# Kernel optimization log

Hardware: AMD Instinct MI355X
Metric: run time of the kernel (lower is better)

## Reference

```python
import jax, jax.numpy as jnp
import numpy as np

N_QUBITS = 10
DEPTH = 2
CNOT_PATTERN = [(i, i + 1) for i in range(N_QUBITS - 1)] + [(N_QUBITS - 1, 0)]

def _signs(n):
    # Pauli-Z eigenvalue (+1/-1) of each basis state for each wire; wire 0 = MSB
    idx = np.arange(2 ** n)
    bits = (idx[:, None] >> np.arange(n - 1, -1, -1)[None, :]) & 1
    return jnp.asarray(1.0 - 2.0 * bits, jnp.float32)  # [2^n, n]

SIGNS = _signs(N_QUBITS)

def _apply_rx(s, theta, wire):
    # s: [B, 2,2,...,2] complex; RX(theta) = [[c, -i s],[-i s, c]], c=cos(theta/2)
    s0 = jnp.take(s, 0, axis=wire + 1)
    s1 = jnp.take(s, 1, axis=wire + 1)
    c = jnp.cos(theta * 0.5)
    sn = jnp.sin(theta * 0.5)
    if c.ndim:  # per-batch angle -> broadcast over remaining wire axes
        shp = (-1,) + (1,) * (s0.ndim - 1)
        c = c.reshape(shp)
        sn = sn.reshape(shp)
    return jnp.stack([c * s0 - 1j * sn * s1, -1j * sn * s0 + c * s1], axis=wire + 1)

def _apply_cnot(s, src, tgt):
    # flip target wire on the src=1 subspace (X gate == flip of the size-2 axis)
    s0 = jnp.take(s, 0, axis=src + 1)
    s1 = jnp.take(s, 1, axis=src + 1)
    t_ax = tgt + 1 - (1 if tgt > src else 0)  # target axis after removing src axis
    s1 = jnp.flip(s1, axis=t_ax)
    return jnp.stack([s0, s1], axis=src + 1)

def _qgate(x, rx_params):
    # x: [B, n_qubits] data angles -> PauliZ expectations [B, n_qubits]
    B = x.shape[0]
    n = N_QUBITS
    s = jnp.zeros((B, 2 ** n), jnp.complex64).at[:, 0].set(1.0)
    s = s.reshape((B,) + (2,) * n)
    for w in range(n):
        s = _apply_rx(s, x[:, w], w)
    for _ in range(DEPTH):
        for w in range(n):
            s = _apply_rx(s, rx_params[w], w)
        for src, tgt in CNOT_PATTERN:
            s = _apply_cnot(s, src, tgt)
    probs = jnp.abs(s.reshape(B, -1)) ** 2  # [B, 2^n]
    return probs @ SIGNS  # [B, n]


def setup_inputs():
    key = jax.random.key(0)
    ks = jax.random.split(key, 10)
    T, B, D, H = 256, 256, 128, N_QUBITS
    fan_in = D + H
    sc = 1.0 / np.sqrt(fan_in)
    def lin(k1, k2):
        W = jax.random.uniform(k1, (H, fan_in), jnp.float32, -sc, sc)
        b = jax.random.uniform(k2, (H,), jnp.float32, -sc, sc)
        return W, b
    inputs = jax.random.normal(ks[0], (T, B, D), jnp.float32)
    rx_params = jax.random.normal(ks[1], (H,), jnp.float32)
    Wf, bf = lin(ks[2], ks[3])
    Wi, bi = lin(ks[4], ks[5])
    Wg, bg = lin(ks[6], ks[7])
    Wo, bo = lin(ks[8], ks[9])
    return dict(inputs=inputs, rx_params=rx_params, Wf=Wf, bf=bf, Wi=Wi, bi=bi,
                Wg=Wg, bg=bg, Wo=Wo, bo=bo)


def reference(inputs, rx_params, Wf, bf, Wi, bi, Wg, bg, Wo, bo):
    T, B, _ = inputs.shape
    H = N_QUBITS
    def step(carry, x_t):
        hx, cx = carry
        comb = jnp.concatenate([x_t, hx], axis=1)  # [B, D+H]
        f = jax.nn.sigmoid(_qgate(comb @ Wf.T + bf, rx_params))
        i = jax.nn.sigmoid(_qgate(comb @ Wi.T + bi, rx_params))
        g = jnp.tanh(_qgate(comb @ Wg.T + bg, rx_params))
        o = jax.nn.sigmoid(_qgate(comb @ Wo.T + bo, rx_params))
        cx = f * cx + i * g
        hx = o * jnp.tanh(cx)
        return (hx, cx), hx
    h0 = jnp.zeros((B, H), inputs.dtype)
    c0 = jnp.zeros((B, H), inputs.dtype)
    (hT, cT), ys = jax.lax.scan(step, (h0, c0), inputs)
    return ys, hT, cT
```

## Files before the change

### kernel.cpp

```cpp
#include <hip/hip_runtime.h>
#include <math.h>

#define T_STEPS 256
#define BATCH   256
#define DDIM    128
#define NH      10

typedef float v2f __attribute__((ext_vector_type(2)));
__device__ __forceinline__ v2f sp(float x){ v2f r; r.x = x; r.y = x; return r; }
#define PKFMA(a,b,c) __builtin_elementwise_fma((a),(b),(c))

template<int CTRL, int RMASK, int BMASK>
__device__ __forceinline__ float dppz(float x){
  return __int_as_float(__builtin_amdgcn_update_dpp(
      0, __float_as_int(x), CTRL, RMASK, BMASK, true));
}
template<int CTRL>
__device__ __forceinline__ float qperm(float x){
  int xi = __float_as_int(x);
  return __int_as_float(__builtin_amdgcn_update_dpp(xi, xi, CTRL, 0xF, 0xF, false));
}
__device__ __forceinline__ float red63(float v){
  v += dppz<0x111, 0xF, 0xF>(v);
  v += dppz<0x112, 0xF, 0xF>(v);
  v += dppz<0x114, 0xF, 0xE>(v);
  v += dppz<0x118, 0xF, 0xC>(v);
  v += dppz<0x142, 0xA, 0xF>(v);
  v += dppz<0x143, 0xC, 0xF>(v);
  return v;
}
__device__ __forceinline__ float rdlane(float v, int l){
  return __int_as_float(__builtin_amdgcn_readlane(__float_as_int(v), l));
}
__device__ __forceinline__ float qp2(float x){ return qperm<0x4E>(x); }
__device__ __forceinline__ float qp1(float x){ return qperm<0xB1>(x); }

template<int CTRL,int RMASK,int BMASK>
__device__ __forceinline__ float lad_add(float v){ return v + dppz<CTRL,RMASK,BMASK>(v); }
template<int CTRL,int RMASK,int BMASK>
__device__ __forceinline__ float lad_sub(float v){ return dppz<CTRL,RMASK,BMASK>(v) - v; }
#define LAD0_A(v) lad_add<0x111,0xF,0xF>(v)
#define LAD0_S(v) lad_sub<0x111,0xF,0xF>(v)
#define LAD1_A(v) lad_add<0x112,0xF,0xF>(v)
#define LAD1_S(v) lad_sub<0x112,0xF,0xF>(v)
#define LAD2_A(v) lad_add<0x114,0xF,0xE>(v)
#define LAD2_S(v) lad_sub<0x114,0xF,0xE>(v)
#define LAD3_A(v) lad_add<0x118,0xF,0xC>(v)
#define LAD3_S(v) lad_sub<0x118,0xF,0xC>(v)
#define LAD4_A(v) lad_add<0x142,0xA,0xF>(v)
#define LAD4_S(v) lad_sub<0x142,0xA,0xF>(v)
#define LAD5_A(v) lad_add<0x143,0xC,0xF>(v)
#define LAD5_S(v) lad_sub<0x143,0xC,0xF>(v)

__device__ __forceinline__ float dsx32(float x){ return __shfl_xor(x, 32, 64); }
__device__ __forceinline__ float dsx16(float x){
  return __int_as_float(__builtin_amdgcn_ds_swizzle(__float_as_int(x), 0x401F));
}
__device__ __forceinline__ float dsx8(float x){
  return __int_as_float(__builtin_amdgcn_ds_swizzle(__float_as_int(x), 0x201F));
}
__device__ __forceinline__ float dsx4(float x){
  return __int_as_float(__builtin_amdgcn_ds_swizzle(__float_as_int(x), 0x101F));
}

#define NK 4

#define RX_LANE_PK(FETCH, cv, sv)                                              \
  { const v2f cc_ = sp(cv), ss_ = sp(sv);                                      \
    _Pragma("unroll")                                                          \
    for (int k = 0; k < NK; ++k){                                              \
      v2f oa, ob;                                                              \
      oa.x = FETCH(RE[k].x); oa.y = FETCH(RE[k].y);                            \
      ob.x = FETCH(IM[k].x); ob.y = FETCH(IM[k].y);                            \
      RE[k] = PKFMA(cc_, RE[k], ss_ * ob);                                     \
      IM[k] = PKFMA(cc_, IM[k], -(ss_ * oa));                                  \
    } }

template<int XB>
__device__ __forceinline__ void rx_reg_pk(float c, float s, v2f* RE, v2f* IM){
  const v2f cc = sp(c), ss = sp(s);
  v2f oR[NK], oI[NK];
  #pragma unroll
  for (int k = 0; k < NK; ++k){ oR[k] = RE[k]; oI[k] = IM[k]; }
  #pragma unroll
  for (int k = 0; k < NK; ++k){
    RE[k] = PKFMA(cc, oR[k],  ss * oI[k ^ XB]);
    IM[k] = PKFMA(cc, oI[k], -(ss * oR[k ^ XB]));
  }
}
__device__ __forceinline__ void rx_reg9_pk(float c, float s, v2f* RE, v2f* IM){
  const v2f cc = sp(c), ss = sp(s);
  #pragma unroll
  for (int k = 0; k < NK; ++k){
    v2f oa = __builtin_shufflevector(RE[k], RE[k], 1, 0);
    v2f ob = __builtin_shufflevector(IM[k], IM[k], 1, 0);
    RE[k] = PKFMA(cc, RE[k],  ss * ob);
    IM[k] = PKFMA(cc, IM[k], -(ss * oa));
  }
}

__device__ __forceinline__ void xdots(float xa, float xb,
                                      const v2f* WA, const v2f* WB, float* s){
  v2f xav = sp(xa), xbv = sp(xb);
  v2f p0 = PKFMA(xav, WA[0], xbv * WB[0]);
  v2f p1 = PKFMA(xav, WA[1], xbv * WB[1]);
  v2f p2 = PKFMA(xav, WA[2], xbv * WB[2]);
  s[0] = red63(p0.x); s[1] = red63(p0.y);
  s[2] = red63(p1.x); s[3] = red63(p1.y);
  s[4] = red63(p2.x);
}

__global__ void __launch_bounds__(512)
__attribute__((amdgpu_waves_per_eu(2)))
qlstm_kernel(const float* __restrict__ inp, const float* __restrict__ rxp,
             const float* __restrict__ Wf, const float* __restrict__ bf,
             const float* __restrict__ Wi, const float* __restrict__ bi,
             const float* __restrict__ Wg, const float* __restrict__ bg,
             const float* __restrict__ Wo, const float* __restrict__ bo,
             float* __restrict__ out)
{
  const int b    = blockIdx.x;
  const int tid  = threadIdx.x;
  const int wv   = tid >> 6;
  const int g    = wv >> 1;
  const int half = wv & 1;
  const int lane = tid & 63;

  __shared__ float4 Sx[4][2][4][64];
  __shared__ float4 partv[2][64];
  __shared__ float xpub_s[4][16];
  ((float*)partv)[tid] = 0.f;

  const float* Wp = (g == 0) ? Wf : (g == 1) ? Wi : (g == 2) ? Wg : Wo;
  const float* bp = (g == 0) ? bf : (g == 1) ? bi : (g == 2) ? bg : bo;

  const float WSC = 0.07957747154594767f;

  const int wbase = half * 5;
  v2f WA[3], WB[3];
  float bq[5];
  #pragma unroll
  for (int k = 0; k < 5; ++k) bq[k] = WSC * (bp[wbase + k] + rxp[wbase + k]);
  #pragma unroll
  for (int j = 0; j < 3; ++j){
    const int w0 = wbase + 2*j, w1 = wbase + 2*j + 1;
    WA[j].x = WSC * Wp[w0*138 + lane];
    WB[j].x = WSC * Wp[w0*138 + 64 + lane];
    if (2*j + 1 < 5){
      WA[j].y = WSC * Wp[w1*138 + lane];
      WB[j].y = WSC * Wp[w1*138 + 64 + lane];
    } else { WA[j].y = 0.f; WB[j].y = 0.f; }
  }
  float wCT[NH];
  {
    const int row = (lane < NH) ? lane : 0;
    #pragma unroll
    for (int j = 0; j < NH; ++j){
      float v = WSC * Wp[row*138 + 128 + j];
      wCT[j] = (lane < NH) ? v : 0.f;
    }
  }

  float pc[NH], ps[NH];
  #pragma unroll
  for (int w = 0; w < NH; ++w){
    float th = 0.5f * rxp[w];
    pc[w] = cosf(th);
    ps[w] = sinf(th);
  }

  const int l5 = (lane>>5)&1, l4 = (lane>>4)&1, l3 = (lane>>3)&1;
  const int l2 = (lane>>2)&1, l1 = (lane>>1)&1, l0 = lane&1;
  const int pb2 = l4^l3, pb3 = l3^l2, pb4 = l2^l1, pb5 = l1^l0;
  const int a0 = l5, a1 = l5^l4;
  const int a6w = l0 ^ half;
  const int n_base = pb2 + pb3 + pb4 + pb5 + a6w;

  v2f CRE[NK], CIM[NK];
  #pragma unroll
  for (int r = 0; r < 2*NK; ++r){
    const int R0 = r&1, R1 = (r>>1)&1, R2 = (r>>2)&1;
    int k = (n_base + (a0^R0) + (a1^R0) + (half^R2) + (R2^R1) + (R1^R0)) & 3;
    float cr = (k==0) ? 1.f : (k==2) ? -1.f : 0.f;
    float ci = (k==1) ? -1.f : (k==3) ? 1.f : 0.f;
    if (R0){ CRE[r>>1].y = cr; CIM[r>>1].y = ci; }
    else   { CRE[r>>1].x = cr; CIM[r>>1].x = ci; }
  }

  const float sig = (lane == 0 || lane >= 6) ? -1.f : 1.f;

  float h = 0.f, c = 0.f;

  const float* x0 = inp + (size_t)b * DDIM;
  float xa = x0[lane];
  float xb = x0[64 + lane];

  {
    float sx[5];
    xdots(xa, xb, WA, WB, sx);
    if (lane == 63){
      #pragma unroll
      for (int k = 0; k < 5; ++k) xpub_s[g][wbase + k] = sx[k] + bq[k];
    }
  }
  __syncthreads();

  #pragma unroll 1
  for (int t = 0; t < T_STEPS; ++t){
    if (t + 1 < T_STEPS){
      const float* nx = inp + ((size_t)(t+1) * BATCH + b) * DDIM;
      xa = nx[lane];
      xb = nx[64 + lane];
    }

    float cs[NH], sn[NH];
    {
      float xr = xpub_s[g][lane & 15];
      float hdA = rdlane(h, 0) * wCT[0];
      float hdB = rdlane(h, 1) * wCT[1];
      hdA = fmaf(rdlane(h, 2), wCT[2], hdA);
      hdB = fmaf(rdlane(h, 3), wCT[3], hdB);
      hdA = fmaf(rdlane(h, 4), wCT[4], hdA);
      hdB = fmaf(rdlane(h, 5), wCT[5], hdB);
      hdA = fmaf(rdlane(h, 6), wCT[6], hdA);
      hdB = fmaf(rdlane(h, 7), wCT[7], hdB);
      hdA = fmaf(rdlane(h, 8), wCT[8], hdA);
      hdB = fmaf(rdlane(h, 9), wCT[9], hdB);
      float th = xr + (hdA + hdB);
      float cA = __builtin_amdgcn_cosf(th);
      float sA = __builtin_amdgcn_sinf(th);
      #pragma unroll
      for (int w = 0; w < NH; ++w){
        cs[w] = rdlane(cA, w);
        sn[w] = rdlane(sA, w);
      }
    }

    float f2 = pb2 ? sn[2] : cs[2];
    float f3 = pb3 ? sn[3] : cs[3];
    float f4 = pb4 ? sn[4] : cs[4];
    float f5 = pb5 ? sn[5] : cs[5];
    float m2345 = ((f2*f3)*(f4*f5)) * (a6w ? sn[6] : cs[6]);

    float q0 = (a0 ? sn[0] : cs[0]) * (a1 ? sn[1] : cs[1]);
    float q1 = (a0 ? cs[0] : sn[0]) * (a1 ? cs[1] : sn[1]);
    v2f ZZ; ZZ.x = m2345 * q0; ZZ.y = m2345 * q1;

    float u7  = half ? sn[7] : cs[7];
    float u7b = half ? cs[7] : sn[7];
    float t78[4];
    t78[0] = u7  * cs[8];
    t78[1] = u7  * sn[8];
    t78[2] = u7b * sn[8];
    t78[3] = u7b * cs[8];

    v2f s9a; s9a.x = cs[9]; s9a.y = sn[9];
    v2f s9b; s9b.x = sn[9]; s9b.y = cs[9];

    v2f RE[NK], IM[NK];
    #pragma unroll
    for (int k = 0; k < NK; ++k){
      v2f M = (sp(t78[k]) * ((k & 1) ? s9b : s9a)) * ZZ;
      RE[k] = M * CRE[k];
      IM[k] = M * CIM[k];
    }

    RX_LANE_PK(dsx32, pc[0], ps[0])
    RX_LANE_PK(dsx16, pc[1], ps[1])
    RX_LANE_PK(dsx8,  pc[2], ps[2])
    RX_LANE_PK(dsx4,  pc[3], ps[3])
    RX_LANE_PK(qp2,   pc[4], ps[4])
    RX_LANE_PK(qp1,   pc[5], ps[5])
    rx_reg_pk<2>(pc[7], ps[7], RE, IM);
    rx_reg_pk<1>(pc[8], ps[8], RE, IM);
    rx_reg9_pk  (pc[9], ps[9], RE, IM);

    Sx[g][half][0][lane] = make_float4(RE[0].x, RE[0].y, RE[1].x, RE[1].y);
    Sx[g][half][1][lane] = make_float4(RE[2].x, RE[2].y, RE[3].x, RE[3].y);
    Sx[g][half][2][lane] = make_float4(IM[0].x, IM[0].y, IM[1].x, IM[1].y);
    Sx[g][half][3][lane] = make_float4(IM[2].x, IM[2].y, IM[3].x, IM[3].y);

    float sx[5];
    xdots(xa, xb, WA, WB, sx);

    __syncthreads();
    {
      float4 pr0 = Sx[g][half^1][0][lane];
      float4 pr1 = Sx[g][half^1][1][lane];
      float4 pi0 = Sx[g][half^1][2][lane];
      float4 pi1 = Sx[g][half^1][3][lane];
      v2f PR[NK], PI[NK];
      PR[0].x = pr0.x; PR[0].y = pr0.y; PR[1].x = pr0.z; PR[1].y = pr0.w;
      PR[2].x = pr1.x; PR[2].y = pr1.y; PR[3].x = pr1.z; PR[3].y = pr1.w;
      PI[0].x = pi0.x; PI[0].y = pi0.y; PI[1].x = pi0.z; PI[1].y = pi0.w;
      PI[2].x = pi1.x; PI[2].y = pi1.y; PI[3].x = pi1.z; PI[3].y = pi1.w;
      const v2f c6 = sp(pc[6]), s6 = sp(ps[6]);
      #pragma unroll
      for (int k = 0; k < NK; ++k){
        RE[k] = PKFMA(c6, RE[k],  s6 * PI[k]);
        IM[k] = PKFMA(c6, IM[k], -(s6 * PR[k]));
      }
    }

    v2f Pk[NK];
    #pragma unroll
    for (int k = 0; k < NK; ++k) Pk[k] = PKFMA(RE[k], RE[k], IM[k] * IM[k]);
    float A0 = Pk[0].x + Pk[0].y, A1 = Pk[1].x + Pk[1].y;
    float A2 = Pk[2].x + Pk[2].y, A3 = Pk[3].x + Pk[3].y;
    float B0 = Pk[0].x - Pk[0].y, B1 = Pk[1].x - Pk[1].y;
    float B2 = Pk[2].x - Pk[2].y, B3 = Pk[3].x - Pk[3].y;
    float su = A0 + A1, sv = A2 + A3;
    float tot = su + sv;
    float q4  = su - sv;
    float q6  = (A0 - A1) - (A2 - A3);
    float q7  = (B0 - B1) - (B2 - B3);

    float a0p = LAD0_A(tot);
    float a0m = LAD0_S(tot);
    float b1pp = LAD1_A(a0p);
    float b1pm = LAD1_S(a0p);
    float b1mm = LAD1_S(a0m);
    float c2ppp = LAD2_A(b1pp);
    float c2ppm = LAD2_S(b1pp);
    float c2pmm = LAD2_S(b1pm);
    float c2mmm = LAD2_S(b1mm);
    float d1 = LAD3_A(c2ppp);
    float d2 = LAD3_S(c2ppp);
    float d3 = LAD3_S(c2ppm);
    float d4 = LAD3_S(c2pmm);
    float d5 = LAD3_S(c2mmm);
    float P1 = LAD5_S(LAD4_S(d1));
    float P2 = LAD5_S(LAD4_S(d2));
    float P3 = LAD5_S(LAD4_S(d3));
    float P4 = LAD5_S(LAD4_S(d4));
    float P5 = LAD5_S(LAD4_S(d5));
    float e = LAD0_S(q7);
    e = LAD1_S(e); e = LAD2_S(e); e = LAD3_S(e); e = LAD4_S(e);
    float P9 = LAD5_S(e);
    float P0 = LAD5_A(e);
    float f_ = LAD0_S(q4);
    f_ = LAD1_S(f_); f_ = LAD2_S(f_); f_ = LAD3_S(f_); f_ = LAD4_S(f_);
    float P7 = LAD5_S(f_);
    float g_ = LAD0_S(q6);
    g_ = LAD1_S(g_); g_ = LAD2_S(g_); g_ = LAD3_S(g_); g_ = LAD4_S(g_);
    float P8 = LAD5_S(g_);

    if (lane == 63){
      float vals[10] = {P0,P1,P2,P3,P4,P5,P5,P7,P8,P9};
      #pragma unroll
      for (int j = 0; j < 10; ++j)
        ((float*)&partv[half][j])[g] = vals[j];
      #pragma unroll
      for (int k = 0; k < 5; ++k)
        xpub_s[g][wbase + k] = sx[k] + bq[k];
    }
    __syncthreads();

    float4 eL = partv[0][lane];
    float4 eH = partv[1][lane];
    float E0 = fmaf(sig, eH.x, eL.x);
    float E1 = fmaf(sig, eH.y, eL.y);
    float E2 = fmaf(sig, eH.z, eL.z);
    float E3 = fmaf(sig, eH.w, eL.w);
    float fv = 1.f / (1.f + __expf(-E0));
    float iv = 1.f / (1.f + __expf(-E1));
    float e2g = __expf(2.f * E2);
    float gv = (e2g - 1.f) / (e2g + 1.f);
    float ov = 1.f / (1.f + __expf(-E3));
    c = fmaf(fv, c, iv * gv);
    float e2c = __expf(2.f * c);
    h = ov * ((e2c - 1.f) / (e2c + 1.f));

    if (wv == 0 && lane < NH)
      out[((size_t)t * BATCH + b) * NH + lane] = h;
  }

  if (wv == 0 && lane < NH){
    const size_t ysN = (size_t)T_STEPS * BATCH * NH;
    out[ysN + (size_t)b * NH + lane]                      = h;
    out[ysN + (size_t)BATCH * NH + (size_t)b * NH + lane] = c;
  }
}

extern "C" void kernel_launch(void* const* d_in, const int* in_sizes, int n_in,
                              void* d_out, int out_size, void* d_ws, size_t ws_size,
                              hipStream_t stream)
{
  qlstm_kernel<<<BATCH, 512, 0, stream>>>(
      (const float*)d_in[0], (const float*)d_in[1],
      (const float*)d_in[2], (const float*)d_in[3],
      (const float*)d_in[4], (const float*)d_in[5],
      (const float*)d_in[6], (const float*)d_in[7],
      (const float*)d_in[8], (const float*)d_in[9],
      (float*)d_out);
}
```

Before: 879.6 us.

## Factor RX cosines into initial state and use tangent-form gate updates

Each RX gate is rewritten as cos*(I - i tan*X). The product of all cosines is folded into the initial state constants, so each gate update becomes a single packed FMA per component instead of a multiply plus an FMA. The DPP quad permutes for wires 4 and 5 are also replaced with ds_swizzle xor-2 and xor-1 operations. The tangent form can blow up or lose accuracy if some cos(theta/2) is near zero, and the swizzles go through the LDS crossbar rather than DPP.

```diff
diff --git a/kernel.cpp b/kernel.cpp
--- a/kernel.cpp
+++ b/kernel.cpp
@@ -14,11 +14,6 @@
 __device__ __forceinline__ float dppz(float x){
   return __int_as_float(__builtin_amdgcn_update_dpp(
       0, __float_as_int(x), CTRL, RMASK, BMASK, true));
-}
-template<int CTRL>
-__device__ __forceinline__ float qperm(float x){
-  int xi = __float_as_int(x);
-  return __int_as_float(__builtin_amdgcn_update_dpp(xi, xi, CTRL, 0xF, 0xF, false));
 }
 __device__ __forceinline__ float red63(float v){
   v += dppz<0x111, 0xF, 0xF>(v);
@@ -32,8 +27,6 @@
 __device__ __forceinline__ float rdlane(float v, int l){
   return __int_as_float(__builtin_amdgcn_readlane(__float_as_int(v), l));
 }
-__device__ __forceinline__ float qp2(float x){ return qperm<0x4E>(x); }
-__device__ __forceinline__ float qp1(float x){ return qperm<0xB1>(x); }
 
 template<int CTRL,int RMASK,int BMASK>
 __device__ __forceinline__ float lad_add(float v){ return v + dppz<CTRL,RMASK,BMASK>(v); }
@@ -62,40 +55,46 @@
 __device__ __forceinline__ float dsx4(float x){
   return __int_as_float(__builtin_amdgcn_ds_swizzle(__float_as_int(x), 0x101F));
 }
+__device__ __forceinline__ float dsx2(float x){
+  return __int_as_float(__builtin_amdgcn_ds_swizzle(__float_as_int(x), 0x081F));
+}
+__device__ __forceinline__ float dsx1(float x){
+  return __int_as_float(__builtin_amdgcn_ds_swizzle(__float_as_int(x), 0x041F));
+}
 
 #define NK 4
 
-#define RX_LANE_PK(FETCH, cv, sv)                                              \
-  { const v2f cc_ = sp(cv), ss_ = sp(sv);                                      \
+#define RX_LANE_T(FETCH, tv)                                                   \
+  { const v2f tt_ = sp(tv), nt_ = sp(-(tv));                                   \
     _Pragma("unroll")                                                          \
     for (int k = 0; k < NK; ++k){                                              \
       v2f oa, ob;                                                              \
       oa.x = FETCH(RE[k].x); oa.y = FETCH(RE[k].y);                            \
       ob.x = FETCH(IM[k].x); ob.y = FETCH(IM[k].y);                            \
-      RE[k] = PKFMA(cc_, RE[k], ss_ * ob);                                     \
-      IM[k] = PKFMA(cc_, IM[k], -(ss_ * oa));                                  \
+      RE[k] = PKFMA(tt_, ob, RE[k]);                                           \
+      IM[k] = PKFMA(nt_, oa, IM[k]);                                           \
     } }
 
 template<int XB>
-__device__ __forceinline__ void rx_reg_pk(float c, float s, v2f* RE, v2f* IM){
-  const v2f cc = sp(c), ss = sp(s);
+__device__ __forceinline__ void rx_reg_t(float tv, v2f* RE, v2f* IM){
+  const v2f tt = sp(tv), nt = sp(-tv);
   v2f oR[NK], oI[NK];
   #pragma unroll
   for (int k = 0; k < NK; ++k){ oR[k] = RE[k]; oI[k] = IM[k]; }
   #pragma unroll
   for (int k = 0; k < NK; ++k){
-    RE[k] = PKFMA(cc, oR[k],  ss * oI[k ^ XB]);
-    IM[k] = PKFMA(cc, oI[k], -(ss * oR[k ^ XB]));
-  }
-}
-__device__ __forceinline__ void rx_reg9_pk(float c, float s, v2f* RE, v2f* IM){
-  const v2f cc = sp(c), ss = sp(s);
+    RE[k] = PKFMA(tt, oI[k ^ XB], RE[k]);
+    IM[k] = PKFMA(nt, oR[k ^ XB], IM[k]);
+  }
+}
+__device__ __forceinline__ void rx_reg9_t(float tv, v2f* RE, v2f* IM){
+  const v2f tt = sp(tv), nt = sp(-tv);
   #pragma unroll
   for (int k = 0; k < NK; ++k){
     v2f oa = __builtin_shufflevector(RE[k], RE[k], 1, 0);
     v2f ob = __builtin_shufflevector(IM[k], IM[k], 1, 0);
-    RE[k] = PKFMA(cc, RE[k],  ss * ob);
-    IM[k] = PKFMA(cc, IM[k], -(ss * oa));
+    RE[k] = PKFMA(tt, ob, RE[k]);
+    IM[k] = PKFMA(nt, oa, IM[k]);
   }
 }
 
@@ -161,12 +160,14 @@
     }
   }
 
-  float pc[NH], ps[NH];
+  float tq[NH];
+  float PC = 1.f;
   #pragma unroll
   for (int w = 0; w < NH; ++w){
     float th = 0.5f * rxp[w];
-    pc[w] = cosf(th);
-    ps[w] = sinf(th);
+    float cw = cosf(th), sw = sinf(th);
+    PC *= cw;
+    tq[w] = sw / cw;
   }
 
   const int l5 = (lane>>5)&1, l4 = (lane>>4)&1, l3 = (lane>>3)&1;
@@ -181,8 +182,8 @@
   for (int r = 0; r < 2*NK; ++r){
     const int R0 = r&1, R1 = (r>>1)&1, R2 = (r>>2)&1;
     int k = (n_base + (a0^R0) + (a1^R0) + (half^R2) + (R2^R1) + (R1^R0)) & 3;
-    float cr = (k==0) ? 1.f : (k==2) ? -1.f : 0.f;
-    float ci = (k==1) ? -1.f : (k==3) ? 1.f : 0.f;
+    float cr = (k==0) ? PC : (k==2) ? -PC : 0.f;
+    float ci = (k==1) ? -PC : (k==3) ? PC : 0.f;
     if (R0){ CRE[r>>1].y = cr; CIM[r>>1].y = ci; }
     else   { CRE[r>>1].x = cr; CIM[r>>1].x = ci; }
   }
@@ -265,15 +266,15 @@
       IM[k] = M * CIM[k];
     }
 
-    RX_LANE_PK(dsx32, pc[0], ps[0])
-    RX_LANE_PK(dsx16, pc[1], ps[1])
-    RX_LANE_PK(dsx8,  pc[2], ps[2])
-    RX_LANE_PK(dsx4,  pc[3], ps[3])
-    RX_LANE_PK(qp2,   pc[4], ps[4])
-    RX_LANE_PK(qp1,   pc[5], ps[5])
-    rx_reg_pk<2>(pc[7], ps[7], RE, IM);
-    rx_reg_pk<1>(pc[8], ps[8], RE, IM);
-    rx_reg9_pk  (pc[9], ps[9], RE, IM);
+    RX_LANE_T(dsx32, tq[0])
+    RX_LANE_T(dsx16, tq[1])
+    RX_LANE_T(dsx8,  tq[2])
+    RX_LANE_T(dsx4,  tq[3])
+    RX_LANE_T(dsx2,  tq[4])
+    RX_LANE_T(dsx1,  tq[5])
+    rx_reg_t<2>(tq[7], RE, IM);
+    rx_reg_t<1>(tq[8], RE, IM);
+    rx_reg9_t  (tq[9], RE, IM);
 
     Sx[g][half][0][lane] = make_float4(RE[0].x, RE[0].y, RE[1].x, RE[1].y);
     Sx[g][half][1][lane] = make_float4(RE[2].x, RE[2].y, RE[3].x, RE[3].y);
@@ -294,11 +295,11 @@
       PR[2].x = pr1.x; PR[2].y = pr1.y; PR[3].x = pr1.z; PR[3].y = pr1.w;
       PI[0].x = pi0.x; PI[0].y = pi0.y; PI[1].x = pi0.z; PI[1].y = pi0.w;
       PI[2].x = pi1.x; PI[2].y = pi1.y; PI[3].x = pi1.z; PI[3].y = pi1.w;
-      const v2f c6 = sp(pc[6]), s6 = sp(ps[6]);
+      const v2f t6 = sp(tq[6]), n6 = sp(-tq[6]);
       #pragma unroll
       for (int k = 0; k < NK; ++k){
-        RE[k] = PKFMA(c6, RE[k],  s6 * PI[k]);
-        IM[k] = PKFMA(c6, IM[k], -(s6 * PR[k]));
+        RE[k] = PKFMA(t6, PI[k], RE[k]);
+        IM[k] = PKFMA(n6, PR[k], IM[k]);
       }
     }
 
```

Measured after the change: 788.8 us. 1.12x faster.
